# Kernel optimization log

Hardware: AMD Instinct MI355X
Metric: run time of the kernel (lower is better)

The kernel has to match this reference:

```python
import jax, jax.numpy as jnp
import numpy as np

E, P, T, B = 512, 128, 1024, 1


def _lstm_dir(x, wih, whh, bih, bhh, reverse):
    # x: [B, T, Din]; torch LSTM gate order: i, f, g, o
    Bb = x.shape[0]
    H = whh.shape[1]
    xg = jnp.einsum('btd,gd->btg', x, wih) + bih + bhh  # [B, T, 4H]
    xg = jnp.swapaxes(xg, 0, 1)  # [T, B, 4H]

    def step(carry, g_t):
        h, c = carry
        g = g_t + h @ whh.T
        i, f, gg, o = jnp.split(g, 4, axis=-1)
        c = jax.nn.sigmoid(f) * c + jax.nn.sigmoid(i) * jnp.tanh(gg)
        h = jax.nn.sigmoid(o) * jnp.tanh(c)
        return (h, c), h

    h0 = jnp.zeros((Bb, H), x.dtype)
    _, hs = jax.lax.scan(step, (h0, h0), xg, reverse=reverse)
    return jnp.swapaxes(hs, 0, 1)  # [B, T, H]


def _bilstm(x, layers):
    for wih, whh, bih, bhh in layers:
        f = _lstm_dir(x, wih[0], whh[0], bih[0], bhh[0], False)
        b = _lstm_dir(x, wih[1], whh[1], bih[1], bhh[1], True)
        x = jnp.concatenate([f, b], axis=-1)
    return x


def setup_inputs() -> dict:
    key = jax.random.key(0)
    ks = jax.random.split(key, 20)
    s = 0.05
    d = {
        'words': jax.random.normal(ks[0], (B, T, E), jnp.float32),
        'pos': jax.random.normal(ks[1], (B, T, P), jnp.float32),
        'w_w0_ih': s * jax.random.normal(ks[2], (2, 4 * E, E), jnp.float32),
        'w_w0_hh': s * jax.random.normal(ks[3], (2, 4 * E, E), jnp.float32),
        'w_b0_ih': s * jax.random.normal(ks[4], (2, 4 * E), jnp.float32),
        'w_b0_hh': s * jax.random.normal(ks[5], (2, 4 * E), jnp.float32),
        'w_w1_ih': s * jax.random.normal(ks[6], (2, 4 * E, 2 * E), jnp.float32),
        'w_w1_hh': s * jax.random.normal(ks[7], (2, 4 * E, E), jnp.float32),
        'w_b1_ih': s * jax.random.normal(ks[8], (2, 4 * E), jnp.float32),
        'w_b1_hh': s * jax.random.normal(ks[9], (2, 4 * E), jnp.float32),
        'p_w0_ih': s * jax.random.normal(ks[10], (2, 4 * P, P), jnp.float32),
        'p_w0_hh': s * jax.random.normal(ks[11], (2, 4 * P, P), jnp.float32),
        'p_b0_ih': s * jax.random.normal(ks[12], (2, 4 * P), jnp.float32),
        'p_b0_hh': s * jax.random.normal(ks[13], (2, 4 * P), jnp.float32),
        'p_w1_ih': s * jax.random.normal(ks[14], (2, 4 * P, 2 * P), jnp.float32),
        'p_w1_hh': s * jax.random.normal(ks[15], (2, 4 * P, P), jnp.float32),
        'p_b1_ih': s * jax.random.normal(ks[16], (2, 4 * P), jnp.float32),
        'p_b1_hh': s * jax.random.normal(ks[17], (2, 4 * P), jnp.float32),
        'edge_w': s * jax.random.normal(ks[18], (1, 4 * (E + P)), jnp.float32),
        'edge_b': s * jax.random.normal(ks[19], (1,), jnp.float32),
    }
    return d


def reference(words, pos, w_w0_ih, w_w0_hh, w_b0_ih, w_b0_hh, w_w1_ih, w_w1_hh,
              w_b1_ih, w_b1_hh, p_w0_ih, p_w0_hh, p_b0_ih, p_b0_hh, p_w1_ih,
              p_w1_hh, p_b1_ih, p_b1_hh, edge_w, edge_b):
    hw = _bilstm(words, [(w_w0_ih, w_w0_hh, w_b0_ih, w_b0_hh),
                         (w_w1_ih, w_w1_hh, w_b1_ih, w_b1_hh)])  # [B,T,2E]
    hp = _bilstm(pos, [(p_w0_ih, p_w0_hh, p_b0_ih, p_b0_hh),
                       (p_w1_ih, p_w1_hh, p_b1_ih, p_b1_hh)])    # [B,T,2P]
    H = jnp.concatenate([hw, hp], axis=-1)[0]  # [T, 2(E+P)]
    D = H.shape[-1]
    # edge_scorer(concat(h_i, h_j)) = h_i @ W1 + h_j @ W2 + b
    s1 = H @ edge_w[0, :D]  # [T]
    s2 = H @ edge_w[0, D:]  # [T]
    S = s1[:, None] + s2[None, :] + edge_b[0]
    n = H.shape[0]
    eye = jnp.eye(n, dtype=bool)
    return jnp.where(eye, jnp.zeros((), S.dtype), S)  # diagonal stays 0
```

## Files before the change

### kernel.cpp

```cpp
#include <hip/hip_runtime.h>


#define T_LEN 1024

__global__ void poison_kernel(unsigned* p, int n) {
  int i = blockIdx.x * blockDim.x + threadIdx.x;
  int stride = gridDim.x * blockDim.x;
  for (; i < n; i += stride) p[i] = 0xFFFFFFFFu;
}

__global__ __launch_bounds__(256) void gemm_bt(
    const float* __restrict__ A,
    const float* __restrict__ Wt,
    const float* __restrict__ B0,
    const float* __restrict__ B1,
    float* __restrict__ C,
    int M, int N, int K)
{
  const int z = blockIdx.z;
  const float* W  = Wt + (size_t)z * N * K;
  const float* b0 = B0 + (size_t)z * N;
  const float* b1 = B1 + (size_t)z * N;
  float* Cz = C + (size_t)z * M * N;

  __shared__ __align__(16) float As[16][64];
  __shared__ __align__(16) float Ws[16][64];

  const int tid = threadIdx.x;
  const int tx = tid & 15, ty = tid >> 4;
  const int brow = blockIdx.y * 64, bcol = blockIdx.x * 64;
  const int lr = tid >> 2;
  const int lk = (tid & 3) << 2;

  float acc[4][4] = {};

  for (int k0 = 0; k0 < K; k0 += 16) {
    float4 av = *(const float4*)(A + (size_t)(brow + lr) * K + k0 + lk);
    float4 wv = *(const float4*)(W + (size_t)(bcol + lr) * K + k0 + lk);
    __syncthreads();
    As[lk + 0][lr] = av.x; As[lk + 1][lr] = av.y;
    As[lk + 2][lr] = av.z; As[lk + 3][lr] = av.w;
    Ws[lk + 0][lr] = wv.x; Ws[lk + 1][lr] = wv.y;
    Ws[lk + 2][lr] = wv.z; Ws[lk + 3][lr] = wv.w;
    __syncthreads();
    #pragma unroll
    for (int kk = 0; kk < 16; ++kk) {
      float4 a = *(const float4*)&As[kk][ty << 2];
      float4 w = *(const float4*)&Ws[kk][tx << 2];
      float a4[4] = {a.x, a.y, a.z, a.w};
      float w4[4] = {w.x, w.y, w.z, w.w};
      #pragma unroll
      for (int i = 0; i < 4; ++i)
        #pragma unroll
        for (int j = 0; j < 4; ++j)
          acc[i][j] = fmaf(a4[i], w4[j], acc[i][j]);
    }
  }

  const int nb = bcol + (tx << 2);
  float bias[4];
  #pragma unroll
  for (int j = 0; j < 4; ++j) bias[j] = b0[nb + j] + b1[nb + j];
  #pragma unroll
  for (int i = 0; i < 4; ++i) {
    int m = brow + (ty << 2) + i;
    float4 out;
    out.x = acc[i][0] + bias[0];
    out.y = acc[i][1] + bias[1];
    out.z = acc[i][2] + bias[2];
    out.w = acc[i][3] + bias[3];
    *(float4*)(Cz + (size_t)m * N + nb) = out;
  }
}

__device__ __forceinline__ float fsigmoid(float x) {
  return 1.f / (1.f + __expf(-x));
}
__device__ __forceinline__ float ftanh(float x) {
  return 2.f / (1.f + __expf(-2.f * x)) - 1.f;
}

__device__ __forceinline__ void word_body(
    int wg, const float* __restrict__ xg, const float* __restrict__ whh,
    float* hbuf, int rev)
{
  const int tid  = threadIdx.x;
  const int r    = tid >> 3;
  const int p    = tid & 7;
  const int gate = r >> 4;
  const int elem = r & 15;
  const int grow = gate * 512 + wg * 16 + elem;

  __shared__ __align__(16) float h_lds[8][68];
  __shared__ float gates[64];

  float w[64];
  #pragma unroll
  for (int c = 0; c < 64; ++c)
    w[c] = whh[(size_t)grow * 512 + p * 64 + c];

  float cstate = 0.f;
  unsigned long long* hb64 = (unsigned long long*)hbuf;
  unsigned* hb32 = (unsigned*)hbuf;

  for (int s = 0; s < T_LEN; ++s) {
    const int t = rev ? (T_LEN - 1 - s) : s;
    const float xgv = xg[(size_t)t * 2048 + grow];

    if (tid < 256) {
      const int f0 = tid << 1;
      float v0, v1;
      if (s == 0) {
        v0 = 0.f; v1 = 0.f;
      } else {
        const int tp = rev ? (t + 1) : (t - 1);
        unsigned long long u = __hip_atomic_load(hb64 + (size_t)tp * 256 + tid,
                                                 __ATOMIC_RELAXED,
                                                 __HIP_MEMORY_SCOPE_AGENT);
        while ((unsigned)u == 0xFFFFFFFFu || (unsigned)(u >> 32) == 0xFFFFFFFFu) {
          u = __hip_atomic_load(hb64 + (size_t)tp * 256 + tid,
                                __ATOMIC_RELAXED, __HIP_MEMORY_SCOPE_AGENT);
        }
        v0 = __uint_as_float((unsigned)u);
        v1 = __uint_as_float((unsigned)(u >> 32));
      }
      h_lds[f0 >> 6][f0 & 63] = v0;
      h_lds[(f0 + 1) >> 6][(f0 + 1) & 63] = v1;
    }
    __syncthreads();

    const float4* h4 = (const float4*)&h_lds[p][0];
    float a0 = 0.f, a1 = 0.f, a2 = 0.f, a3 = 0.f;
    #pragma unroll
    for (int c4 = 0; c4 < 16; ++c4) {
      float4 hv = h4[c4];
      a0 = fmaf(w[4 * c4 + 0], hv.x, a0);
      a1 = fmaf(w[4 * c4 + 1], hv.y, a1);
      a2 = fmaf(w[4 * c4 + 2], hv.z, a2);
      a3 = fmaf(w[4 * c4 + 3], hv.w, a3);
    }
    float acc = (a0 + a1) + (a2 + a3);
    acc += __shfl_xor(acc, 1, 64);
    acc += __shfl_xor(acc, 2, 64);
    acc += __shfl_xor(acc, 4, 64);
    if (p == 0) gates[r] = acc + xgv;
    __syncthreads();

    if (tid < 16) {
      float si = fsigmoid(gates[tid]);
      float sf = fsigmoid(gates[16 + tid]);
      float tg = ftanh(gates[32 + tid]);
      float so = fsigmoid(gates[48 + tid]);
      cstate = fmaf(sf, cstate, si * tg);
      float h = so * ftanh(cstate);
      __hip_atomic_store(hb32 + (size_t)t * 512 + wg * 16 + tid,
                         __float_as_uint(h),
                         __ATOMIC_RELAXED, __HIP_MEMORY_SCOPE_AGENT);
    }
  }
}

__device__ __forceinline__ void pos_body(
    const float* __restrict__ xg, const float* __restrict__ whh,
    float* __restrict__ hbuf, int rev)
{
  const int tid = threadIdx.x;

  __shared__ __align__(16) float h_lds[128];
  __shared__ float gates[512];

  float w[128];
  #pragma unroll
  for (int c = 0; c < 128; ++c)
    w[c] = whh[(size_t)tid * 128 + c];

  float cstate = 0.f;

  for (int s = 0; s < T_LEN; ++s) {
    const int t = rev ? (T_LEN - 1 - s) : s;
    const float xgv = xg[(size_t)t * 512 + tid];

    if (s == 0 && tid < 128) h_lds[tid] = 0.f;
    __syncthreads();

    const float4* h4 = (const float4*)&h_lds[0];
    float a0 = 0.f, a1 = 0.f, a2 = 0.f, a3 = 0.f;
    #pragma unroll
    for (int c4 = 0; c4 < 32; ++c4) {
      float4 hv = h4[c4];
      a0 = fmaf(w[4 * c4 + 0], hv.x, a0);
      a1 = fmaf(w[4 * c4 + 1], hv.y, a1);
      a2 = fmaf(w[4 * c4 + 2], hv.z, a2);
      a3 = fmaf(w[4 * c4 + 3], hv.w, a3);
    }
    gates[tid] = ((a0 + a1) + (a2 + a3)) + xgv;
    __syncthreads();

    if (tid < 128) {
      float si = fsigmoid(gates[tid]);
      float sf = fsigmoid(gates[128 + tid]);
      float tg = ftanh(gates[256 + tid]);
      float so = fsigmoid(gates[384 + tid]);
      cstate = fmaf(sf, cstate, si * tg);
      float h = so * ftanh(cstate);
      h_lds[tid] = h;
      hbuf[(size_t)t * 128 + tid] = h;
    }
  }
}

__global__ __launch_bounds__(512, 1) void rec_kernel(
    const float* xg_wf, const float* xg_wb, const float* whh_w,
    float* h_wf, float* h_wb,
    const float* xg_pf, const float* xg_pb, const float* whh_p,
    float* h_pf, float* h_pb)
{
  int b = blockIdx.x;
  if (b < 32)        word_body(b,      xg_wf, whh_w,             h_wf, 0);
  else if (b < 64)   word_body(b - 32, xg_wb, whh_w + 2048 * 512, h_wb, 1);
  else if (b == 64)  pos_body(xg_pf, whh_p,             h_pf, 0);
  else               pos_body(xg_pb, whh_p + 512 * 128, h_pb, 1);
}

__global__ void concat_k(const float* __restrict__ wf, const float* __restrict__ wb,
                         const float* __restrict__ pf, const float* __restrict__ pb,
                         float* __restrict__ wcat, float* __restrict__ pcat)
{
  const int totw = T_LEN * 1024;
  const int totp = T_LEN * 256;
  int idx = blockIdx.x * blockDim.x + threadIdx.x;
  int stride = gridDim.x * blockDim.x;
  for (int e = idx; e < totw + totp; e += stride) {
    if (e < totw) {
      int t = e >> 10, d = e & 1023;
      wcat[e] = d < 512 ? wf[t * 512 + d] : wb[t * 512 + (d - 512)];
    } else {
      int e2 = e - totw;
      int t = e2 >> 8, d = e2 & 255;
      pcat[e2] = d < 128 ? pf[t * 128 + d] : pb[t * 128 + (d - 128)];
    }
  }
}

__global__ __launch_bounds__(256) void edge_s(
    const float* __restrict__ hwf, const float* __restrict__ hwb,
    const float* __restrict__ hpf, const float* __restrict__ hpb,
    const float* __restrict__ ew, float* s1, float* s2)
{
  const int i = blockIdx.x;
  const int tid = threadIdx.x;
  float a1 = 0.f, a2 = 0.f;
  for (int d = tid; d < 1280; d += 256) {
    float hv;
    if (d < 512)       hv = hwf[i * 512 + d];
    else if (d < 1024) hv = hwb[i * 512 + d - 512];
    else if (d < 1152) hv = hpf[i * 128 + d - 1024];
    else               hv = hpb[i * 128 + d - 1152];
    a1 = fmaf(hv, ew[d], a1);
    a2 = fmaf(hv, ew[1280 + d], a2);
  }
  #pragma unroll
  for (int off = 32; off > 0; off >>= 1) {
    a1 += __shfl_xor(a1, off, 64);
    a2 += __shfl_xor(a2, off, 64);
  }
  __shared__ float r1[4], r2[4];
  const int wid = tid >> 6;
  if ((tid & 63) == 0) { r1[wid] = a1; r2[wid] = a2; }
  __syncthreads();
  if (tid == 0) {
    s1[i] = (r1[0] + r1[1]) + (r1[2] + r1[3]);
    s2[i] = (r2[0] + r2[1]) + (r2[2] + r2[3]);
  }
}

__global__ __launch_bounds__(256) void sfill(
    const float* __restrict__ s1, const float* __restrict__ s2,
    const float* __restrict__ eb, float* __restrict__ out)
{
  int e = blockIdx.x * 256 + threadIdx.x;
  int i = e >> 10, j = e & 1023;
  out[e] = (i == j) ? 0.f : s1[i] + s2[j] + eb[0];
}

extern "C" void kernel_launch(void* const* d_in, const int* in_sizes, int n_in,
                              void* d_out, int out_size, void* d_ws, size_t ws_size,
                              hipStream_t stream)
{
  const float* words   = (const float*)d_in[0];
  const float* pos     = (const float*)d_in[1];
  const float* w_w0_ih = (const float*)d_in[2];
  const float* w_w0_hh = (const float*)d_in[3];
  const float* w_b0_ih = (const float*)d_in[4];
  const float* w_b0_hh = (const float*)d_in[5];
  const float* w_w1_ih = (const float*)d_in[6];
  const float* w_w1_hh = (const float*)d_in[7];
  const float* w_b1_ih = (const float*)d_in[8];
  const float* w_b1_hh = (const float*)d_in[9];
  const float* p_w0_ih = (const float*)d_in[10];
  const float* p_w0_hh = (const float*)d_in[11];
  const float* p_b0_ih = (const float*)d_in[12];
  const float* p_b0_hh = (const float*)d_in[13];
  const float* p_w1_ih = (const float*)d_in[14];
  const float* p_w1_hh = (const float*)d_in[15];
  const float* p_b1_ih = (const float*)d_in[16];
  const float* p_b1_hh = (const float*)d_in[17];
  const float* edge_w  = (const float*)d_in[18];
  const float* edge_b  = (const float*)d_in[19];

  float* ws = (float*)d_ws;
  float* xg_w  = ws;
  float* xg_p  = ws + 4194304;
  float* hw0_f = ws + 5242880;
  float* hw0_b = hw0_f + 524288;
  float* hw1_f = hw0_b + 524288;
  float* hw1_b = hw1_f + 524288;
  float* hp0_f = hw1_b + 524288;
  float* hp0_b = hp0_f + 131072;
  float* hp1_f = hp0_b + 131072;
  float* hp1_b = hp1_f + 131072;
  float* wcat  = hp1_b + 131072;
  float* pcat  = wcat + 1048576;
  float* s1    = pcat + 262144;
  float* s2    = s1 + 1024;

  poison_kernel<<<1024, 256, 0, stream>>>((unsigned*)hw0_f, 2097152);

  gemm_bt<<<dim3(32, 16, 2), 256, 0, stream>>>(words, w_w0_ih, w_b0_ih, w_b0_hh,
                                               xg_w, 1024, 2048, 512);
  gemm_bt<<<dim3(8, 16, 2), 256, 0, stream>>>(pos, p_w0_ih, p_b0_ih, p_b0_hh,
                                              xg_p, 1024, 512, 128);

  rec_kernel<<<66, 512, 0, stream>>>(xg_w, xg_w + 2097152, w_w0_hh, hw0_f, hw0_b,
                                     xg_p, xg_p + 524288, p_w0_hh, hp0_f, hp0_b);

  concat_k<<<2048, 256, 0, stream>>>(hw0_f, hw0_b, hp0_f, hp0_b, wcat, pcat);

  gemm_bt<<<dim3(32, 16, 2), 256, 0, stream>>>(wcat, w_w1_ih, w_b1_ih, w_b1_hh,
                                               xg_w, 1024, 2048, 1024);
  gemm_bt<<<dim3(8, 16, 2), 256, 0, stream>>>(pcat, p_w1_ih, p_b1_ih, p_b1_hh,
                                              xg_p, 1024, 512, 256);

  rec_kernel<<<66, 512, 0, stream>>>(xg_w, xg_w + 2097152, w_w1_hh, hw1_f, hw1_b,
                                     xg_p, xg_p + 524288, p_w1_hh, hp1_f, hp1_b);

  edge_s<<<1024, 256, 0, stream>>>(hw1_f, hw1_b, hp1_f, hp1_b, edge_w, s1, s2);
  sfill<<<4096, 256, 0, stream>>>(s1, s2, edge_b, (float*)d_out);
}
```

Baseline: 3.453 ms.

## Merge forward and backward word LSTM directions into one workgroup per slice

Each word-LSTM workgroup now runs both the forward and the backward recurrence for its 16-element hidden slice. The two directions' matvecs, shuffles and gate math are interleaved, so the grid drops from 66 to 34 workgroups. The next step's input-gate value is also prefetched one iteration ahead so its load overlaps the current step. The aim is to overlap the two independent dependency chains inside one wave schedule and to cut the number of spinning workgroups. In exchange it doubles register use for weights (128 floats per thread) and lengthens per-step work, and each step may now wait on the slower of the two directions.

```diff
diff --git a/kernel.cpp b/kernel.cpp
--- a/kernel.cpp
+++ b/kernel.cpp
@@ -80,9 +80,15 @@
   return 2.f / (1.f + __expf(-2.f * x)) - 1.f;
 }
 
+__device__ __forceinline__ bool hpoison(unsigned long long u) {
+  return ((unsigned)u == 0xFFFFFFFFu) || ((unsigned)(u >> 32) == 0xFFFFFFFFu);
+}
+
 __device__ __forceinline__ void word_body(
-    int wg, const float* __restrict__ xg, const float* __restrict__ whh,
-    float* hbuf, int rev)
+    int wg,
+    const float* __restrict__ xg_f, const float* __restrict__ xg_b,
+    const float* __restrict__ whh_f, const float* __restrict__ whh_b,
+    float* hbuf_f, float* hbuf_b)
 {
   const int tid  = threadIdx.x;
   const int r    = tid >> 3;
@@ -91,72 +97,127 @@
   const int elem = r & 15;
   const int grow = gate * 512 + wg * 16 + elem;
 
-  __shared__ __align__(16) float h_lds[8][68];
-  __shared__ float gates[64];
-
-  float w[64];
+  __shared__ __align__(16) float h_f[8][68];
+  __shared__ __align__(16) float h_b[8][68];
+  __shared__ float gatesF[64];
+  __shared__ float gatesB[64];
+
+  float wf[64], wb[64];
   #pragma unroll
-  for (int c = 0; c < 64; ++c)
-    w[c] = whh[(size_t)grow * 512 + p * 64 + c];
-
-  float cstate = 0.f;
-  unsigned long long* hb64 = (unsigned long long*)hbuf;
-  unsigned* hb32 = (unsigned*)hbuf;
+  for (int c = 0; c < 64; ++c) {
+    wf[c] = whh_f[(size_t)grow * 512 + p * 64 + c];
+    wb[c] = whh_b[(size_t)grow * 512 + p * 64 + c];
+  }
+
+  float cst = 0.f;
+  unsigned long long* f64p = (unsigned long long*)hbuf_f;
+  unsigned long long* b64p = (unsigned long long*)hbuf_b;
+  unsigned* f32p = (unsigned*)hbuf_f;
+  unsigned* b32p = (unsigned*)hbuf_b;
+
+  float xgf = 0.f, xgb = 0.f;
+  if (p == 0) {
+    xgf = xg_f[grow];
+    xgb = xg_b[(size_t)(T_LEN - 1) * 2048 + grow];
+  }
 
   for (int s = 0; s < T_LEN; ++s) {
-    const int t = rev ? (T_LEN - 1 - s) : s;
-    const float xgv = xg[(size_t)t * 2048 + grow];
-
-    if (tid < 256) {
-      const int f0 = tid << 1;
-      float v0, v1;
+    const int t  = s;
+    const int tb = T_LEN - 1 - s;
+
+    if (tid >= 256) {
+      const int g  = tid - 256;
+      const int f0 = g << 1;
+      float v0, v1, u0, u1;
       if (s == 0) {
-        v0 = 0.f; v1 = 0.f;
+        v0 = v1 = u0 = u1 = 0.f;
       } else {
-        const int tp = rev ? (t + 1) : (t - 1);
-        unsigned long long u = __hip_atomic_load(hb64 + (size_t)tp * 256 + tid,
-                                                 __ATOMIC_RELAXED,
-                                                 __HIP_MEMORY_SCOPE_AGENT);
-        while ((unsigned)u == 0xFFFFFFFFu || (unsigned)(u >> 32) == 0xFFFFFFFFu) {
-          u = __hip_atomic_load(hb64 + (size_t)tp * 256 + tid,
-                                __ATOMIC_RELAXED, __HIP_MEMORY_SCOPE_AGENT);
-        }
-        v0 = __uint_as_float((unsigned)u);
-        v1 = __uint_as_float((unsigned)(u >> 32));
+        unsigned long long uf = __hip_atomic_load(
+            f64p + (size_t)(s - 1) * 256 + g,
+            __ATOMIC_RELAXED, __HIP_MEMORY_SCOPE_AGENT);
+        unsigned long long ub = __hip_atomic_load(
+            b64p + (size_t)(T_LEN - s) * 256 + g,
+            __ATOMIC_RELAXED, __HIP_MEMORY_SCOPE_AGENT);
+        while (hpoison(uf))
+          uf = __hip_atomic_load(f64p + (size_t)(s - 1) * 256 + g,
+                                 __ATOMIC_RELAXED, __HIP_MEMORY_SCOPE_AGENT);
+        while (hpoison(ub))
+          ub = __hip_atomic_load(b64p + (size_t)(T_LEN - s) * 256 + g,
+                                 __ATOMIC_RELAXED, __HIP_MEMORY_SCOPE_AGENT);
+        v0 = __uint_as_float((unsigned)uf);
+        v1 = __uint_as_float((unsigned)(uf >> 32));
+        u0 = __uint_as_float((unsigned)ub);
+        u1 = __uint_as_float((unsigned)(ub >> 32));
       }
-      h_lds[f0 >> 6][f0 & 63] = v0;
-      h_lds[(f0 + 1) >> 6][(f0 + 1) & 63] = v1;
-    }
-    __syncthreads();
-
-    const float4* h4 = (const float4*)&h_lds[p][0];
-    float a0 = 0.f, a1 = 0.f, a2 = 0.f, a3 = 0.f;
+      h_f[f0 >> 6][f0 & 63] = v0;
+      h_f[(f0 + 1) >> 6][(f0 + 1) & 63] = v1;
+      h_b[f0 >> 6][f0 & 63] = u0;
+      h_b[(f0 + 1) >> 6][(f0 + 1) & 63] = u1;
+    }
+    __syncthreads();
+
+    float xgf_n = 0.f, xgb_n = 0.f;
+    if (p == 0 && s + 1 < T_LEN) {
+      xgf_n = xg_f[(size_t)(s + 1) * 2048 + grow];
+      xgb_n = xg_b[(size_t)(T_LEN - 2 - s) * 2048 + grow];
+    }
+
+    const float4* hf4 = (const float4*)&h_f[p][0];
+    const float4* hb4 = (const float4*)&h_b[p][0];
+    float fa0 = 0.f, fa1 = 0.f, fa2 = 0.f, fa3 = 0.f;
+    float ba0 = 0.f, ba1 = 0.f, ba2 = 0.f, ba3 = 0.f;
     #pragma unroll
     for (int c4 = 0; c4 < 16; ++c4) {
-      float4 hv = h4[c4];
-      a0 = fmaf(w[4 * c4 + 0], hv.x, a0);
-      a1 = fmaf(w[4 * c4 + 1], hv.y, a1);
-      a2 = fmaf(w[4 * c4 + 2], hv.z, a2);
-      a3 = fmaf(w[4 * c4 + 3], hv.w, a3);
-    }
-    float acc = (a0 + a1) + (a2 + a3);
-    acc += __shfl_xor(acc, 1, 64);
-    acc += __shfl_xor(acc, 2, 64);
-    acc += __shfl_xor(acc, 4, 64);
-    if (p == 0) gates[r] = acc + xgv;
-    __syncthreads();
-
-    if (tid < 16) {
-      float si = fsigmoid(gates[tid]);
-      float sf = fsigmoid(gates[16 + tid]);
-      float tg = ftanh(gates[32 + tid]);
-      float so = fsigmoid(gates[48 + tid]);
-      cstate = fmaf(sf, cstate, si * tg);
-      float h = so * ftanh(cstate);
-      __hip_atomic_store(hb32 + (size_t)t * 512 + wg * 16 + tid,
-                         __float_as_uint(h),
-                         __ATOMIC_RELAXED, __HIP_MEMORY_SCOPE_AGENT);
-    }
+      float4 hv = hf4[c4];
+      float4 kv = hb4[c4];
+      fa0 = fmaf(wf[4 * c4 + 0], hv.x, fa0);
+      fa1 = fmaf(wf[4 * c4 + 1], hv.y, fa1);
+      fa2 = fmaf(wf[4 * c4 + 2], hv.z, fa2);
+      fa3 = fmaf(wf[4 * c4 + 3], hv.w, fa3);
+      ba0 = fmaf(wb[4 * c4 + 0], kv.x, ba0);
+      ba1 = fmaf(wb[4 * c4 + 1], kv.y, ba1);
+      ba2 = fmaf(wb[4 * c4 + 2], kv.z, ba2);
+      ba3 = fmaf(wb[4 * c4 + 3], kv.w, ba3);
+    }
+    float accf = (fa0 + fa1) + (fa2 + fa3);
+    float accb = (ba0 + ba1) + (ba2 + ba3);
+    accf += __shfl_xor(accf, 1, 64);
+    accb += __shfl_xor(accb, 1, 64);
+    accf += __shfl_xor(accf, 2, 64);
+    accb += __shfl_xor(accb, 2, 64);
+    accf += __shfl_xor(accf, 4, 64);
+    accb += __shfl_xor(accb, 4, 64);
+    if (p == 0) {
+      gatesF[r] = accf + xgf;
+      gatesB[r] = accb + xgb;
+    }
+    __syncthreads();
+
+    if (tid < 32) {
+      const bool isB = tid >= 16;
+      const int  e   = tid & 15;
+      const float* gb = isB ? gatesB : gatesF;
+      float gi = gb[e];
+      float gf = gb[16 + e];
+      float gg = gb[32 + e];
+      float go = gb[48 + e];
+      float si = fsigmoid(gi);
+      float sf = fsigmoid(gf);
+      float tg = ftanh(gg);
+      float so = fsigmoid(go);
+      cst = fmaf(sf, cst, si * tg);
+      float h = so * ftanh(cst);
+      if (!isB)
+        __hip_atomic_store(f32p + (size_t)t * 512 + wg * 16 + e,
+                           __float_as_uint(h),
+                           __ATOMIC_RELAXED, __HIP_MEMORY_SCOPE_AGENT);
+      else
+        __hip_atomic_store(b32p + (size_t)tb * 512 + wg * 16 + e,
+                           __float_as_uint(h),
+                           __ATOMIC_RELAXED, __HIP_MEMORY_SCOPE_AGENT);
+    }
+    xgf = xgf_n;
+    xgb = xgb_n;
   }
 }
 
@@ -216,10 +277,12 @@
     float* h_pf, float* h_pb)
 {
   int b = blockIdx.x;
-  if (b < 32)        word_body(b,      xg_wf, whh_w,             h_wf, 0);
-  else if (b < 64)   word_body(b - 32, xg_wb, whh_w + 2048 * 512, h_wb, 1);
-  else if (b == 64)  pos_body(xg_pf, whh_p,             h_pf, 0);
-  else               pos_body(xg_pb, whh_p + 512 * 128, h_pb, 1);
+  if (b < 32)
+    word_body(b, xg_wf, xg_wb, whh_w, whh_w + 2048 * 512, h_wf, h_wb);
+  else if (b == 32)
+    pos_body(xg_pf, whh_p, h_pf, 0);
+  else
+    pos_body(xg_pb, whh_p + 512 * 128, h_pb, 1);
 }
 
 __global__ void concat_k(const float* __restrict__ wf, const float* __restrict__ wb,
@@ -331,7 +394,7 @@
   gemm_bt<<<dim3(8, 16, 2), 256, 0, stream>>>(pos, p_w0_ih, p_b0_ih, p_b0_hh,
                                               xg_p, 1024, 512, 128);
 
-  rec_kernel<<<66, 512, 0, stream>>>(xg_w, xg_w + 2097152, w_w0_hh, hw0_f, hw0_b,
+  rec_kernel<<<34, 512, 0, stream>>>(xg_w, xg_w + 2097152, w_w0_hh, hw0_f, hw0_b,
                                      xg_p, xg_p + 524288, p_w0_hh, hp0_f, hp0_b);
 
   concat_k<<<2048, 256, 0, stream>>>(hw0_f, hw0_b, hp0_f, hp0_b, wcat, pcat);
@@ -341,7 +404,7 @@
   gemm_bt<<<dim3(8, 16, 2), 256, 0, stream>>>(pcat, p_w1_ih, p_b1_ih, p_b1_hh,
                                               xg_p, 1024, 512, 256);
 
-  rec_kernel<<<66, 512, 0, stream>>>(xg_w, xg_w + 2097152, w_w1_hh, hw1_f, hw1_b,
+  rec_kernel<<<34, 512, 0, stream>>>(xg_w, xg_w + 2097152, w_w1_hh, hw1_f, hw1_b,
                                      xg_p, xg_p + 524288, p_w1_hh, hp1_f, hp1_b);
 
   edge_s<<<1024, 256, 0, stream>>>(hw1_f, hw1_b, hp1_f, hp1_b, edge_w, s1, s2);
```

New measurement: 4.751 ms. 37.6% more time.

## Restructure word LSTM recurrence to per-wave gates without LDS barriers

Applied to the files above, without the earlier changes.

Reorganizes the word-direction recurrent step so each half-wave owns one hidden element and computes all four gates. Every lane polls the previous hidden state straight from global memory with vectorized cache-bypassing loads, then reduces the gate sums with shuffles. This removes both __syncthreads barriers and the LDS staging per timestep, and prefetches the next step's input-gate values one step ahead. The cost is many more redundant global polling loads, since every half-wave reads the full 512-element h vector, plus reliance on inline asm cache bits for coherence.

```diff
diff --git a/kernel.cpp b/kernel.cpp
--- a/kernel.cpp
+++ b/kernel.cpp
@@ -2,6 +2,8 @@
 
 
 #define T_LEN 1024
+
+typedef unsigned uint4v __attribute__((ext_vector_type(4)));
 
 __global__ void poison_kernel(unsigned* p, int n) {
   int i = blockIdx.x * blockDim.x + threadIdx.x;
@@ -80,83 +82,129 @@
   return 2.f / (1.f + __expf(-2.f * x)) - 1.f;
 }
 
+__device__ __forceinline__ bool vpoison(uint4v v) {
+  return v[0] == 0xFFFFFFFFu || v[1] == 0xFFFFFFFFu ||
+         v[2] == 0xFFFFFFFFu || v[3] == 0xFFFFFFFFu;
+}
+
+__device__ __forceinline__ uint4v respin(uint4v v, const unsigned* addr) {
+  while (vpoison(v)) {
+    asm volatile("global_load_dwordx4 %0, %1, off sc0 sc1\n\t"
+                 "s_waitcnt vmcnt(0)"
+                 : "=&v"(v) : "v"(addr) : "memory");
+  }
+  return v;
+}
+
 __device__ __forceinline__ void word_body(
     int wg, const float* __restrict__ xg, const float* __restrict__ whh,
     float* hbuf, int rev)
 {
   const int tid  = threadIdx.x;
-  const int r    = tid >> 3;
-  const int p    = tid & 7;
-  const int gate = r >> 4;
-  const int elem = r & 15;
-  const int grow = gate * 512 + wg * 16 + elem;
-
-  __shared__ __align__(16) float h_lds[8][68];
-  __shared__ float gates[64];
-
-  float w[64];
+  const int wave = tid >> 6;
+  const int lane = tid & 63;
+  const int half = lane >> 5;
+  const int p    = lane & 31;
+  const int e    = wg * 16 + wave * 2 + half;
+
+  float w[4][16];
   #pragma unroll
-  for (int c = 0; c < 64; ++c)
-    w[c] = whh[(size_t)grow * 512 + p * 64 + c];
-
-  float cstate = 0.f;
-  unsigned long long* hb64 = (unsigned long long*)hbuf;
-  unsigned* hb32 = (unsigned*)hbuf;
+  for (int g = 0; g < 4; ++g) {
+    const float* row = whh + ((size_t)(g * 512 + e)) * 512 + p * 16;
+    #pragma unroll
+    for (int c4 = 0; c4 < 4; ++c4) {
+      float4 v = *(const float4*)(row + 4 * c4);
+      w[g][4 * c4 + 0] = v.x; w[g][4 * c4 + 1] = v.y;
+      w[g][4 * c4 + 2] = v.z; w[g][4 * c4 + 3] = v.w;
+    }
+  }
+
+  unsigned* hb = (unsigned*)hbuf;
+  float cst = 0.f;
+
+  float xg4[4];
+  {
+    const int t0 = rev ? (T_LEN - 1) : 0;
+    #pragma unroll
+    for (int g = 0; g < 4; ++g)
+      xg4[g] = xg[(size_t)t0 * 2048 + g * 512 + e];
+  }
 
   for (int s = 0; s < T_LEN; ++s) {
     const int t = rev ? (T_LEN - 1 - s) : s;
-    const float xgv = xg[(size_t)t * 2048 + grow];
-
-    if (tid < 256) {
-      const int f0 = tid << 1;
-      float v0, v1;
-      if (s == 0) {
-        v0 = 0.f; v1 = 0.f;
-      } else {
-        const int tp = rev ? (t + 1) : (t - 1);
-        unsigned long long u = __hip_atomic_load(hb64 + (size_t)tp * 256 + tid,
-                                                 __ATOMIC_RELAXED,
-                                                 __HIP_MEMORY_SCOPE_AGENT);
-        while ((unsigned)u == 0xFFFFFFFFu || (unsigned)(u >> 32) == 0xFFFFFFFFu) {
-          u = __hip_atomic_load(hb64 + (size_t)tp * 256 + tid,
-                                __ATOMIC_RELAXED, __HIP_MEMORY_SCOPE_AGENT);
-        }
-        v0 = __uint_as_float((unsigned)u);
-        v1 = __uint_as_float((unsigned)(u >> 32));
+
+    float hv[16];
+    if (s == 0) {
+      #pragma unroll
+      for (int i = 0; i < 16; ++i) hv[i] = 0.f;
+    } else {
+      const int tp = rev ? (t + 1) : (t - 1);
+      const unsigned* b0 = hb + (size_t)tp * 512 + p * 16;
+      const unsigned* b1 = b0 + 4;
+      const unsigned* b2 = b0 + 8;
+      const unsigned* b3 = b0 + 12;
+      uint4v va, vb, vc, vd;
+      asm volatile(
+          "global_load_dwordx4 %0, %4, off sc0 sc1\n\t"
+          "global_load_dwordx4 %1, %5, off sc0 sc1\n\t"
+          "global_load_dwordx4 %2, %6, off sc0 sc1\n\t"
+          "global_load_dwordx4 %3, %7, off sc0 sc1\n\t"
+          "s_waitcnt vmcnt(0)"
+          : "=&v"(va), "=&v"(vb), "=&v"(vc), "=&v"(vd)
+          : "v"(b0), "v"(b1), "v"(b2), "v"(b3)
+          : "memory");
+      va = respin(va, b0);
+      vb = respin(vb, b1);
+      vc = respin(vc, b2);
+      vd = respin(vd, b3);
+      #pragma unroll
+      for (int i = 0; i < 4; ++i) {
+        hv[i]      = __uint_as_float(va[i]);
+        hv[4 + i]  = __uint_as_float(vb[i]);
+        hv[8 + i]  = __uint_as_float(vc[i]);
+        hv[12 + i] = __uint_as_float(vd[i]);
       }
-      h_lds[f0 >> 6][f0 & 63] = v0;
-      h_lds[(f0 + 1) >> 6][(f0 + 1) & 63] = v1;
-    }
-    __syncthreads();
-
-    const float4* h4 = (const float4*)&h_lds[p][0];
+    }
+
     float a0 = 0.f, a1 = 0.f, a2 = 0.f, a3 = 0.f;
     #pragma unroll
-    for (int c4 = 0; c4 < 16; ++c4) {
-      float4 hv = h4[c4];
-      a0 = fmaf(w[4 * c4 + 0], hv.x, a0);
-      a1 = fmaf(w[4 * c4 + 1], hv.y, a1);
-      a2 = fmaf(w[4 * c4 + 2], hv.z, a2);
-      a3 = fmaf(w[4 * c4 + 3], hv.w, a3);
-    }
-    float acc = (a0 + a1) + (a2 + a3);
-    acc += __shfl_xor(acc, 1, 64);
-    acc += __shfl_xor(acc, 2, 64);
-    acc += __shfl_xor(acc, 4, 64);
-    if (p == 0) gates[r] = acc + xgv;
-    __syncthreads();
-
-    if (tid < 16) {
-      float si = fsigmoid(gates[tid]);
-      float sf = fsigmoid(gates[16 + tid]);
-      float tg = ftanh(gates[32 + tid]);
-      float so = fsigmoid(gates[48 + tid]);
-      cstate = fmaf(sf, cstate, si * tg);
-      float h = so * ftanh(cstate);
-      __hip_atomic_store(hb32 + (size_t)t * 512 + wg * 16 + tid,
-                         __float_as_uint(h),
+    for (int c = 0; c < 16; ++c) {
+      a0 = fmaf(w[0][c], hv[c], a0);
+      a1 = fmaf(w[1][c], hv[c], a1);
+      a2 = fmaf(w[2][c], hv[c], a2);
+      a3 = fmaf(w[3][c], hv[c], a3);
+    }
+
+    float xgn[4];
+    if (s + 1 < T_LEN) {
+      const int tn = rev ? (t - 1) : (t + 1);
+      #pragma unroll
+      for (int g = 0; g < 4; ++g)
+        xgn[g] = xg[(size_t)tn * 2048 + g * 512 + e];
+    } else {
+      xgn[0] = xgn[1] = xgn[2] = xgn[3] = 0.f;
+    }
+
+    #pragma unroll
+    for (int k = 1; k <= 16; k <<= 1) {
+      a0 += __shfl_xor(a0, k, 64);
+      a1 += __shfl_xor(a1, k, 64);
+      a2 += __shfl_xor(a2, k, 64);
+      a3 += __shfl_xor(a3, k, 64);
+    }
+
+    float si = fsigmoid(a0 + xg4[0]);
+    float sf = fsigmoid(a1 + xg4[1]);
+    float tg = ftanh  (a2 + xg4[2]);
+    float so = fsigmoid(a3 + xg4[3]);
+    cst = fmaf(sf, cst, si * tg);
+    float h = so * ftanh(cst);
+
+    if (p == 0)
+      __hip_atomic_store(hb + (size_t)t * 512 + e, __float_as_uint(h),
                          __ATOMIC_RELAXED, __HIP_MEMORY_SCOPE_AGENT);
-    }
+
+    xg4[0] = xgn[0]; xg4[1] = xgn[1]; xg4[2] = xgn[2]; xg4[3] = xgn[3];
   }
 }
 
@@ -216,10 +264,14 @@
     float* h_pf, float* h_pb)
 {
   int b = blockIdx.x;
-  if (b < 32)        word_body(b,      xg_wf, whh_w,             h_wf, 0);
-  else if (b < 64)   word_body(b - 32, xg_wb, whh_w + 2048 * 512, h_wb, 1);
-  else if (b == 64)  pos_body(xg_pf, whh_p,             h_pf, 0);
-  else               pos_body(xg_pb, whh_p + 512 * 128, h_pb, 1);
+  if (b < 32)
+    word_body(b, xg_wf, whh_w, h_wf, 0);
+  else if (b < 64)
+    word_body(b - 32, xg_wb, whh_w + 2048 * 512, h_wb, 1);
+  else if (b == 64)
+    pos_body(xg_pf, whh_p, h_pf, 0);
+  else
+    pos_body(xg_pb, whh_p + 512 * 128, h_pb, 1);
 }
 
 __global__ void concat_k(const float* __restrict__ wf, const float* __restrict__ wb,
```

Result: slower. 10.48 ms (+203.4%).
